# Performance work log

Measured on AMD Instinct MI355X. Metric: run time of the kernel, lower is better.

Reference implementation:

```python
import jax, jax.numpy as jnp
import numpy as np

EPS = 1e-3  # keras BatchNormalization default epsilon

def _spatial_shift(x):
    # x: [B, T, N, C]; channel c is circularly rolled along N by (c % N)
    B, T, N, C = x.shape
    shifts = np.arange(C) % N                      # [C]
    pos = np.arange(N)[:, None]                    # [N,1]
    # tf.roll(shift=s) moves element j to (j+s) % N, i.e. out[j] = in[(j - s) % N]
    gather_idx = (pos - shifts[None, :]) % N       # [N, C]
    return x[:, :, gather_idx, np.arange(C)]       # advanced indexing -> [B,T,N,C]

def setup_inputs() -> dict:
    key = jax.random.key(0)
    k1, k2, k3 = jax.random.split(key, 3)
    B, T, N, C_in, F = 8, 64, 21, 128, 256
    x = jax.random.normal(k1, (B, T, N, C_in), dtype=jnp.float32)
    W = jax.random.normal(k2, (C_in, F), dtype=jnp.float32) * (1.0 / np.sqrt(C_in))
    b = jnp.zeros((F,), dtype=jnp.float32)
    gamma = jnp.ones((F,), dtype=jnp.float32)
    beta = jnp.zeros((F,), dtype=jnp.float32)
    return {"x": x, "W": W, "b": b, "gamma": gamma, "beta": beta}

def reference(x, W, b, gamma, beta):
    # per-channel circular shift along N
    xs = _spatial_shift(x)                               # [B,T,N,C]
    # 1x1 conv == matmul over channel dim
    y = jnp.einsum('btnc,cf->btnf', xs, W) + b           # [B,T,N,F]
    # BatchNormalization with training=True: batch statistics over B,T,N
    mean = jnp.mean(y, axis=(0, 1, 2))
    var = jnp.var(y, axis=(0, 1, 2))
    y = (y - mean) * jax.lax.rsqrt(var + EPS) * gamma + beta
    return jax.nn.relu(y)
```

## Files before the change

### kernel.cpp

```cpp
#include <hip/hip_runtime.h>
#include <stdint.h>


#define NPOS 21
#define CIN  128
#define FOUT 256
#define BT   512
#define M_TOTAL 10752
#define BN_EPS 1e-3f
#define AROW 136

typedef short v8s __attribute__((ext_vector_type(8)));
typedef float v4f __attribute__((ext_vector_type(4)));

__device__ __forceinline__ uint16_t f2bf_rne(float f) {
    uint32_t u = __builtin_bit_cast(uint32_t, f);
    u += 0x7FFFu + ((u >> 16) & 1u);
    return (uint16_t)(u >> 16);
}

__global__ __launch_bounds__(256) void k_prep(const float* __restrict__ W,
                                              float* __restrict__ ws)
{
    const int t = threadIdx.x;
    if (blockIdx.x == 0) { ws[t] = 0.0f; ws[256 + t] = 0.0f; }

    uint4* dst = (uint4*)(ws + 1024);
    #pragma unroll
    for (int it = 0; it < 4; it++) {
        int q   = (blockIdx.x * 4 + it) * 256 + t;
        int l   = q & 63;
        int ks  = (q >> 6) & 3;
        int nt  = q >> 8;
        int kb  = ks * 32 + (l >> 4) * 8;
        int col = nt * 16 + (l & 15);
        uint32_t d[4];
        #pragma unroll
        for (int p = 0; p < 4; p++) {
            uint32_t lo = f2bf_rne(W[(size_t)(kb + 2 * p    ) * FOUT + col]);
            uint32_t hi = f2bf_rne(W[(size_t)(kb + 2 * p + 1) * FOUT + col]);
            d[p] = lo | (hi << 16);
        }
        dst[q] = make_uint4(d[0], d[1], d[2], d[3]);
    }
}

__global__ __launch_bounds__(256) void k_conv(const float* __restrict__ x,
                                              float* __restrict__ y,
                                              float* ws)
{
    __shared__ uint16_t asB[32 * AROW];
    __shared__ float sumL[FOUT], sqL[FOUT];

    const int bt = blockIdx.x;
    const int t  = threadIdx.x;

    for (int i = t; i < 704; i += 256) {
        int r  = 21 + (i >> 6);
        int c2 = (i & 63) << 1;
        *(uint32_t*)&asB[r * AROW + c2] = 0u;
    }
    const float* xin = x + (size_t)bt * (NPOS * CIN);
    for (int i = t; i < NPOS * CIN; i += 256) {
        float v = xin[i];
        int r = i >> 7;
        int c = i & (CIN - 1);
        int s = c % NPOS;
        int n = r + s; if (n >= NPOS) n -= NPOS;
        asB[n * AROW + c] = f2bf_rne(v);
    }
    __syncthreads();

    const int w     = t >> 6;
    const int l     = t & 63;
    const int row16 = l & 15;
    const int koct  = l >> 4;

    const uint4* wsw = (const uint4*)(ws + 1024);
    v8s bfr[4][4];
    #pragma unroll
    for (int nt = 0; nt < 4; nt++)
        #pragma unroll
        for (int ks = 0; ks < 4; ks++) {
            uint4 u = wsw[(((w * 4 + nt) * 4 + ks) << 6) + l];
            bfr[nt][ks] = __builtin_bit_cast(v8s, u);
        }

    float s4[4] = {0.f, 0.f, 0.f, 0.f};
    float q4[4] = {0.f, 0.f, 0.f, 0.f};
    float* yout = y + (size_t)bt * (NPOS * FOUT) + w * 64;

    #pragma unroll
    for (int m = 0; m < 2; m++) {
        v8s afr[4];
        #pragma unroll
        for (int ks = 0; ks < 4; ks++)
            afr[ks] = *(const v8s*)&asB[(m * 16 + row16) * AROW + ks * 32 + koct * 8];

        v4f acc[4];
        #pragma unroll
        for (int nt = 0; nt < 4; nt++) acc[nt] = (v4f){0.f, 0.f, 0.f, 0.f};

        #pragma unroll
        for (int ks = 0; ks < 4; ks++)
            #pragma unroll
            for (int nt = 0; nt < 4; nt++)
                acc[nt] = __builtin_amdgcn_mfma_f32_16x16x32_bf16(
                              afr[ks], bfr[nt][ks], acc[nt], 0, 0, 0);

        #pragma unroll
        for (int nt = 0; nt < 4; nt++) {
            #pragma unroll
            for (int rg = 0; rg < 4; rg++) {
                float v = acc[nt][rg];
                int gr = m * 16 + koct * 4 + rg;
                if (gr < NPOS)
                    yout[(size_t)gr * FOUT + nt * 16 + row16] = v;
                s4[nt] += v;
                q4[nt] += v * v;
            }
        }
    }

    #pragma unroll
    for (int nt = 0; nt < 4; nt++) {
        float s = s4[nt], q = q4[nt];
        s += __shfl_xor(s, 16); s += __shfl_xor(s, 32);
        q += __shfl_xor(q, 16); q += __shfl_xor(q, 32);
        if (l < 16) {
            sumL[w * 64 + nt * 16 + l] = s;
            sqL [w * 64 + nt * 16 + l] = q;
        }
    }
    __syncthreads();
    atomicAdd(ws + t, sumL[t]);
    atomicAdd(ws + FOUT + t, sqL[t]);
}

#define BN_BLOCKS 1344

__global__ __launch_bounds__(256) void k_bnapply(float* __restrict__ y,
                                                 const float* __restrict__ ws,
                                                 const float* __restrict__ gamma,
                                                 const float* __restrict__ beta)
{
    const int t  = threadIdx.x;
    const int fb = (t & 63) << 2;
    const float4 sm = *(const float4*)(ws + fb);
    const float4 sq = *(const float4*)(ws + FOUT + fb);
    const float4 gm = *(const float4*)(gamma + fb);
    const float4 be = *(const float4*)(beta + fb);
    const float invM = 1.0f / (float)M_TOTAL;

    float sc[4], bs[4];
    {
        float m0 = sm.x * invM, m1 = sm.y * invM, m2 = sm.z * invM, m3 = sm.w * invM;
        float v0 = fmaf(-m0, m0, sq.x * invM);
        float v1 = fmaf(-m1, m1, sq.y * invM);
        float v2 = fmaf(-m2, m2, sq.z * invM);
        float v3 = fmaf(-m3, m3, sq.w * invM);
        sc[0] = rsqrtf(v0 + BN_EPS) * gm.x;  bs[0] = be.x - m0 * sc[0];
        sc[1] = rsqrtf(v1 + BN_EPS) * gm.y;  bs[1] = be.y - m1 * sc[1];
        sc[2] = rsqrtf(v2 + BN_EPS) * gm.z;  bs[2] = be.z - m2 * sc[2];
        sc[3] = rsqrtf(v3 + BN_EPS) * gm.w;  bs[3] = be.w - m3 * sc[3];
    }

    float4* y4 = (float4*)y;
    #pragma unroll
    for (int it = 0; it < 2; it++) {
        int g = blockIdx.x * 512 + it * 256 + t;
        float4 v = y4[g];
        v.x = fmaxf(fmaf(v.x, sc[0], bs[0]), 0.0f);
        v.y = fmaxf(fmaf(v.y, sc[1], bs[1]), 0.0f);
        v.z = fmaxf(fmaf(v.z, sc[2], bs[2]), 0.0f);
        v.w = fmaxf(fmaf(v.w, sc[3], bs[3]), 0.0f);
        y4[g] = v;
    }
}

extern "C" __global__ void SpatialShiftConvBlock_71923522339050_kernel() {}

extern "C" void kernel_launch(void* const* d_in, const int* in_sizes, int n_in,
                              void* d_out, int out_size, void* d_ws, size_t ws_size,
                              hipStream_t stream) {
    float* y  = (float*)d_out;
    float* ws = (float*)d_ws;
    k_prep<<<4, 256, 0, stream>>>((const float*)d_in[1], ws);
    k_conv<<<BT, 256, 0, stream>>>((const float*)d_in[0], y, ws);
    k_bnapply<<<BN_BLOCKS, 256, 0, stream>>>(y, ws,
                                             (const float*)d_in[3], (const float*)d_in[4]);
}
```

Measured before the change: 91.37 us.

## Fuse conv, batch-stat reduction and BN apply into one kernel with grid barrier

Merges the weight prep, conv and BN-apply kernels into a single kernel. Each block converts W to bf16 fragments directly from global memory, keeps its conv accumulators in registers, and publishes partial sums via atomics. A software grid-wide barrier (atomic counter spin) then lets every block read the global statistics and write normalized ReLU output once. This removes the intermediate y write/read round-trip and two launches, but relies on all 512 blocks being co-resident and duplicates the W conversion in every block.

Measured after the change: 125.6 us. +37.5%, slower.

```diff
diff --git a/kernel.cpp b/kernel.cpp
--- a/kernel.cpp
+++ b/kernel.cpp
@@ -19,38 +19,16 @@
     return (uint16_t)(u >> 16);
 }
 
-__global__ __launch_bounds__(256) void k_prep(const float* __restrict__ W,
-                                              float* __restrict__ ws)
-{
-    const int t = threadIdx.x;
-    if (blockIdx.x == 0) { ws[t] = 0.0f; ws[256 + t] = 0.0f; }
-
-    uint4* dst = (uint4*)(ws + 1024);
-    #pragma unroll
-    for (int it = 0; it < 4; it++) {
-        int q   = (blockIdx.x * 4 + it) * 256 + t;
-        int l   = q & 63;
-        int ks  = (q >> 6) & 3;
-        int nt  = q >> 8;
-        int kb  = ks * 32 + (l >> 4) * 8;
-        int col = nt * 16 + (l & 15);
-        uint32_t d[4];
-        #pragma unroll
-        for (int p = 0; p < 4; p++) {
-            uint32_t lo = f2bf_rne(W[(size_t)(kb + 2 * p    ) * FOUT + col]);
-            uint32_t hi = f2bf_rne(W[(size_t)(kb + 2 * p + 1) * FOUT + col]);
-            d[p] = lo | (hi << 16);
-        }
-        dst[q] = make_uint4(d[0], d[1], d[2], d[3]);
-    }
-}
-
-__global__ __launch_bounds__(256) void k_conv(const float* __restrict__ x,
-                                              float* __restrict__ y,
-                                              float* ws)
+__global__ __launch_bounds__(256, 2) void k_fused(const float* __restrict__ x,
+                                                  const float* __restrict__ W,
+                                                  const float* __restrict__ gamma,
+                                                  const float* __restrict__ beta,
+                                                  float* __restrict__ y,
+                                                  float* ws)
 {
     __shared__ uint16_t asB[32 * AROW];
-    __shared__ float sumL[FOUT], sqL[FOUT];
+    __shared__ float scL[FOUT];
+    __shared__ float bsL[FOUT];
 
     const int bt = blockIdx.x;
     const int t  = threadIdx.x;
@@ -69,26 +47,37 @@
         int n = r + s; if (n >= NPOS) n -= NPOS;
         asB[n * AROW + c] = f2bf_rne(v);
     }
-    __syncthreads();
 
     const int w     = t >> 6;
     const int l     = t & 63;
     const int row16 = l & 15;
     const int koct  = l >> 4;
 
-    const uint4* wsw = (const uint4*)(ws + 1024);
     v8s bfr[4][4];
     #pragma unroll
-    for (int nt = 0; nt < 4; nt++)
+    for (int nt = 0; nt < 4; nt++) {
+        const int col = (w * 4 + nt) * 16 + row16;
         #pragma unroll
         for (int ks = 0; ks < 4; ks++) {
-            uint4 u = wsw[(((w * 4 + nt) * 4 + ks) << 6) + l];
+            const int kb = ks * 32 + koct * 8;
+            uint32_t d[4];
+            #pragma unroll
+            for (int p = 0; p < 4; p++) {
+                uint32_t lo = f2bf_rne(W[(size_t)(kb + 2 * p    ) * FOUT + col]);
+                uint32_t hi = f2bf_rne(W[(size_t)(kb + 2 * p + 1) * FOUT + col]);
+                d[p] = lo | (hi << 16);
+            }
+            uint4 u = make_uint4(d[0], d[1], d[2], d[3]);
             bfr[nt][ks] = __builtin_bit_cast(v8s, u);
         }
+    }
+    __syncthreads();
 
-    float s4[4] = {0.f, 0.f, 0.f, 0.f};
-    float q4[4] = {0.f, 0.f, 0.f, 0.f};
-    float* yout = y + (size_t)bt * (NPOS * FOUT) + w * 64;
+    v4f acc[2][4];
+    #pragma unroll
+    for (int m = 0; m < 2; m++)
+        #pragma unroll
+        for (int nt = 0; nt < 4; nt++) acc[m][nt] = (v4f){0.f, 0.f, 0.f, 0.f};
 
     #pragma unroll
     for (int m = 0; m < 2; m++) {
@@ -96,85 +85,75 @@
         #pragma unroll
         for (int ks = 0; ks < 4; ks++)
             afr[ks] = *(const v8s*)&asB[(m * 16 + row16) * AROW + ks * 32 + koct * 8];
-
-        v4f acc[4];
-        #pragma unroll
-        for (int nt = 0; nt < 4; nt++) acc[nt] = (v4f){0.f, 0.f, 0.f, 0.f};
-
         #pragma unroll
         for (int ks = 0; ks < 4; ks++)
             #pragma unroll
             for (int nt = 0; nt < 4; nt++)
-                acc[nt] = __builtin_amdgcn_mfma_f32_16x16x32_bf16(
-                              afr[ks], bfr[nt][ks], acc[nt], 0, 0, 0);
-
-        #pragma unroll
-        for (int nt = 0; nt < 4; nt++) {
-            #pragma unroll
-            for (int rg = 0; rg < 4; rg++) {
-                float v = acc[nt][rg];
-                int gr = m * 16 + koct * 4 + rg;
-                if (gr < NPOS)
-                    yout[(size_t)gr * FOUT + nt * 16 + row16] = v;
-                s4[nt] += v;
-                q4[nt] += v * v;
-            }
-        }
+                acc[m][nt] = __builtin_amdgcn_mfma_f32_16x16x32_bf16(
+                                 afr[ks], bfr[nt][ks], acc[m][nt], 0, 0, 0);
     }
 
     #pragma unroll
     for (int nt = 0; nt < 4; nt++) {
-        float s = s4[nt], q = q4[nt];
+        float s = 0.f, q = 0.f;
+        #pragma unroll
+        for (int m = 0; m < 2; m++)
+            #pragma unroll
+            for (int rg = 0; rg < 4; rg++) {
+                float v = acc[m][nt][rg];
+                s += v; q += v * v;
+            }
         s += __shfl_xor(s, 16); s += __shfl_xor(s, 32);
         q += __shfl_xor(q, 16); q += __shfl_xor(q, 32);
         if (l < 16) {
-            sumL[w * 64 + nt * 16 + l] = s;
-            sqL [w * 64 + nt * 16 + l] = q;
+            scL[w * 64 + nt * 16 + l] = s;
+            bsL[w * 64 + nt * 16 + l] = q;
         }
     }
     __syncthreads();
-    atomicAdd(ws + t, sumL[t]);
-    atomicAdd(ws + FOUT + t, sqL[t]);
-}
+    atomicAdd(ws + t, scL[t]);
+    atomicAdd(ws + FOUT + t, bsL[t]);
+    __threadfence();
+    __syncthreads();
 
-#define BN_BLOCKS 1344
+    if (t == 0) {
+        atomicAdd((unsigned int*)(ws + 512), 1u);
+        while (__hip_atomic_load((unsigned int*)(ws + 512),
+                                 __ATOMIC_RELAXED, __HIP_MEMORY_SCOPE_AGENT)
+               < (unsigned int)gridDim.x)
+            __builtin_amdgcn_s_sleep(2);
+    }
+    __syncthreads();
 
-__global__ __launch_bounds__(256) void k_bnapply(float* __restrict__ y,
-                                                 const float* __restrict__ ws,
-                                                 const float* __restrict__ gamma,
-                                                 const float* __restrict__ beta)
-{
-    const int t  = threadIdx.x;
-    const int fb = (t & 63) << 2;
-    const float4 sm = *(const float4*)(ws + fb);
-    const float4 sq = *(const float4*)(ws + FOUT + fb);
-    const float4 gm = *(const float4*)(gamma + fb);
-    const float4 be = *(const float4*)(beta + fb);
-    const float invM = 1.0f / (float)M_TOTAL;
+    {
+        float s = __hip_atomic_load(ws + t, __ATOMIC_RELAXED,
+                                    __HIP_MEMORY_SCOPE_AGENT);
+        float q = __hip_atomic_load(ws + FOUT + t, __ATOMIC_RELAXED,
+                                    __HIP_MEMORY_SCOPE_AGENT);
+        const float invM = 1.0f / (float)M_TOTAL;
+        float mean = s * invM;
+        float var  = fmaf(-mean, mean, q * invM);
+        float sc   = rsqrtf(var + BN_EPS) * gamma[t];
+        scL[t] = sc;
+        bsL[t] = beta[t] - mean * sc;
+    }
+    __syncthreads();
 
-    float sc[4], bs[4];
-    {
-        float m0 = sm.x * invM, m1 = sm.y * invM, m2 = sm.z * invM, m3 = sm.w * invM;
-        float v0 = fmaf(-m0, m0, sq.x * invM);
-        float v1 = fmaf(-m1, m1, sq.y * invM);
-        float v2 = fmaf(-m2, m2, sq.z * invM);
-        float v3 = fmaf(-m3, m3, sq.w * invM);
-        sc[0] = rsqrtf(v0 + BN_EPS) * gm.x;  bs[0] = be.x - m0 * sc[0];
-        sc[1] = rsqrtf(v1 + BN_EPS) * gm.y;  bs[1] = be.y - m1 * sc[1];
-        sc[2] = rsqrtf(v2 + BN_EPS) * gm.z;  bs[2] = be.z - m2 * sc[2];
-        sc[3] = rsqrtf(v3 + BN_EPS) * gm.w;  bs[3] = be.w - m3 * sc[3];
-    }
-
-    float4* y4 = (float4*)y;
+    float* yout = y + (size_t)bt * (NPOS * FOUT);
     #pragma unroll
-    for (int it = 0; it < 2; it++) {
-        int g = blockIdx.x * 512 + it * 256 + t;
-        float4 v = y4[g];
-        v.x = fmaxf(fmaf(v.x, sc[0], bs[0]), 0.0f);
-        v.y = fmaxf(fmaf(v.y, sc[1], bs[1]), 0.0f);
-        v.z = fmaxf(fmaf(v.z, sc[2], bs[2]), 0.0f);
-        v.w = fmaxf(fmaf(v.w, sc[3], bs[3]), 0.0f);
-        y4[g] = v;
+    for (int nt = 0; nt < 4; nt++) {
+        const int ch = w * 64 + nt * 16 + row16;
+        const float sc = scL[ch];
+        const float bs = bsL[ch];
+        #pragma unroll
+        for (int m = 0; m < 2; m++)
+            #pragma unroll
+            for (int rg = 0; rg < 4; rg++) {
+                int gr = m * 16 + koct * 4 + rg;
+                if (gr < NPOS)
+                    yout[(size_t)gr * FOUT + ch] =
+                        fmaxf(fmaf(acc[m][nt][rg], sc, bs), 0.0f);
+            }
     }
 }
 
@@ -185,8 +164,8 @@
                               hipStream_t stream) {
     float* y  = (float*)d_out;
     float* ws = (float*)d_ws;
-    k_prep<<<4, 256, 0, stream>>>((const float*)d_in[1], ws);
-    k_conv<<<BT, 256, 0, stream>>>((const float*)d_in[0], y, ws);
-    k_bnapply<<<BN_BLOCKS, 256, 0, stream>>>(y, ws,
-                                             (const float*)d_in[3], (const float*)d_in[4]);
+    hipMemsetAsync(ws, 0, 516 * sizeof(float), stream);
+    k_fused<<<BT, 256, 0, stream>>>((const float*)d_in[0], (const float*)d_in[1],
+                                    (const float*)d_in[3], (const float*)d_in[4],
+                                    y, ws);
 }
```

## Split conv output features across two blocks per row group and widen prep grid

Applied to the files above, without the earlier changes.

The conv kernel now launches two blocks per (b,t) slice, each computing half of the 256 output features, so each wave holds fewer B fragments. This doubles grid parallelism on a 256-CU device. In exchange, the shifted input tile is loaded and converted twice. The weight-prep kernel uses 16 blocks with one fragment per thread instead of 4 blocks looping, and the B-fragment loads are moved ahead of the LDS barrier to overlap with the input staging. Atomics per block are halved, though the total number of atomics stays the same.

Measured after the change: 91.41 us. Within noise of the previous version (+0.0%).

```diff
diff --git a/kernel.cpp b/kernel.cpp
--- a/kernel.cpp
+++ b/kernel.cpp
@@ -9,6 +9,7 @@
 #define M_TOTAL 10752
 #define BN_EPS 1e-3f
 #define AROW 136
+#define WSFRAG 1024
 
 typedef short v8s __attribute__((ext_vector_type(8)));
 typedef float v4f __attribute__((ext_vector_type(4)));
@@ -23,26 +24,23 @@
                                               float* __restrict__ ws)
 {
     const int t = threadIdx.x;
-    if (blockIdx.x == 0) { ws[t] = 0.0f; ws[256 + t] = 0.0f; }
+    const int b = blockIdx.x;
+    if (b < 2) ws[b * 256 + t] = 0.0f;
 
-    uint4* dst = (uint4*)(ws + 1024);
+    const int q  = b * 256 + t;
+    const int l  = q & 63;
+    const int ks = (q >> 6) & 3;
+    const int nt = q >> 8;
+    const int kb = ks * 32 + (l >> 4) * 8;
+    const int col = nt * 16 + (l & 15);
+    uint32_t d[4];
     #pragma unroll
-    for (int it = 0; it < 4; it++) {
-        int q   = (blockIdx.x * 4 + it) * 256 + t;
-        int l   = q & 63;
-        int ks  = (q >> 6) & 3;
-        int nt  = q >> 8;
-        int kb  = ks * 32 + (l >> 4) * 8;
-        int col = nt * 16 + (l & 15);
-        uint32_t d[4];
-        #pragma unroll
-        for (int p = 0; p < 4; p++) {
-            uint32_t lo = f2bf_rne(W[(size_t)(kb + 2 * p    ) * FOUT + col]);
-            uint32_t hi = f2bf_rne(W[(size_t)(kb + 2 * p + 1) * FOUT + col]);
-            d[p] = lo | (hi << 16);
-        }
-        dst[q] = make_uint4(d[0], d[1], d[2], d[3]);
+    for (int p = 0; p < 4; p++) {
+        uint32_t lo = f2bf_rne(W[(size_t)(kb + 2 * p    ) * FOUT + col]);
+        uint32_t hi = f2bf_rne(W[(size_t)(kb + 2 * p + 1) * FOUT + col]);
+        d[p] = lo | (hi << 16);
     }
+    ((uint4*)(ws + WSFRAG))[q] = make_uint4(d[0], d[1], d[2], d[3]);
 }
 
 __global__ __launch_bounds__(256) void k_conv(const float* __restrict__ x,
@@ -50,9 +48,10 @@
                                               float* ws)
 {
     __shared__ uint16_t asB[32 * AROW];
-    __shared__ float sumL[FOUT], sqL[FOUT];
+    __shared__ float scL[128], sqL[128];
 
-    const int bt = blockIdx.x;
+    const int bt = blockIdx.x >> 1;
+    const int fh = blockIdx.x & 1;
     const int t  = threadIdx.x;
 
     for (int i = t; i < 704; i += 256) {
@@ -69,26 +68,30 @@
         int n = r + s; if (n >= NPOS) n -= NPOS;
         asB[n * AROW + c] = f2bf_rne(v);
     }
-    __syncthreads();
 
     const int w     = t >> 6;
     const int l     = t & 63;
     const int row16 = l & 15;
     const int koct  = l >> 4;
 
-    const uint4* wsw = (const uint4*)(ws + 1024);
-    v8s bfr[4][4];
+    const uint4* wsw = (const uint4*)(ws + WSFRAG);
+    v8s bfr[2][4];
     #pragma unroll
-    for (int nt = 0; nt < 4; nt++)
+    for (int nt = 0; nt < 2; nt++) {
+        const int ntg = fh * 8 + w * 2 + nt;
         #pragma unroll
         for (int ks = 0; ks < 4; ks++) {
-            uint4 u = wsw[(((w * 4 + nt) * 4 + ks) << 6) + l];
+            uint4 u = wsw[(((ntg << 2) + ks) << 6) + l];
             bfr[nt][ks] = __builtin_bit_cast(v8s, u);
         }
+    }
+    __syncthreads();
 
-    float s4[4] = {0.f, 0.f, 0.f, 0.f};
-    float q4[4] = {0.f, 0.f, 0.f, 0.f};
-    float* yout = y + (size_t)bt * (NPOS * FOUT) + w * 64;
+    v4f acc[2][2];
+    #pragma unroll
+    for (int m = 0; m < 2; m++)
+        #pragma unroll
+        for (int nt = 0; nt < 2; nt++) acc[m][nt] = (v4f){0.f, 0.f, 0.f, 0.f};
 
     #pragma unroll
     for (int m = 0; m < 2; m++) {
@@ -96,45 +99,39 @@
         #pragma unroll
         for (int ks = 0; ks < 4; ks++)
             afr[ks] = *(const v8s*)&asB[(m * 16 + row16) * AROW + ks * 32 + koct * 8];
-
-        v4f acc[4];
-        #pragma unroll
-        for (int nt = 0; nt < 4; nt++) acc[nt] = (v4f){0.f, 0.f, 0.f, 0.f};
-
         #pragma unroll
         for (int ks = 0; ks < 4; ks++)
             #pragma unroll
-            for (int nt = 0; nt < 4; nt++)
-                acc[nt] = __builtin_amdgcn_mfma_f32_16x16x32_bf16(
-                              afr[ks], bfr[nt][ks], acc[nt], 0, 0, 0);
+            for (int nt = 0; nt < 2; nt++)
+                acc[m][nt] = __builtin_amdgcn_mfma_f32_16x16x32_bf16(
+                                 afr[ks], bfr[nt][ks], acc[m][nt], 0, 0, 0);
+    }
 
+    float* yout = y + (size_t)bt * (NPOS * FOUT) + fh * 128 + w * 32;
+    #pragma unroll
+    for (int nt = 0; nt < 2; nt++) {
+        float s = 0.f, q = 0.f;
         #pragma unroll
-        for (int nt = 0; nt < 4; nt++) {
+        for (int m = 0; m < 2; m++)
             #pragma unroll
             for (int rg = 0; rg < 4; rg++) {
-                float v = acc[nt][rg];
+                float v = acc[m][nt][rg];
+                s += v; q += v * v;
                 int gr = m * 16 + koct * 4 + rg;
                 if (gr < NPOS)
                     yout[(size_t)gr * FOUT + nt * 16 + row16] = v;
-                s4[nt] += v;
-                q4[nt] += v * v;
             }
-        }
-    }
-
-    #pragma unroll
-    for (int nt = 0; nt < 4; nt++) {
-        float s = s4[nt], q = q4[nt];
         s += __shfl_xor(s, 16); s += __shfl_xor(s, 32);
         q += __shfl_xor(q, 16); q += __shfl_xor(q, 32);
         if (l < 16) {
-            sumL[w * 64 + nt * 16 + l] = s;
-            sqL [w * 64 + nt * 16 + l] = q;
+            scL[w * 32 + nt * 16 + l] = s;
+            sqL[w * 32 + nt * 16 + l] = q;
         }
     }
     __syncthreads();
-    atomicAdd(ws + t, sumL[t]);
-    atomicAdd(ws + FOUT + t, sqL[t]);
+
+    if (t < 128) atomicAdd(ws + fh * 128 + t, scL[t]);
+    else         atomicAdd(ws + 256 + fh * 128 + (t - 128), sqL[t - 128]);
 }
 
 #define BN_BLOCKS 1344
@@ -185,8 +182,8 @@
                               hipStream_t stream) {
     float* y  = (float*)d_out;
     float* ws = (float*)d_ws;
-    k_prep<<<4, 256, 0, stream>>>((const float*)d_in[1], ws);
-    k_conv<<<BT, 256, 0, stream>>>((const float*)d_in[0], y, ws);
+    k_prep<<<16, 256, 0, stream>>>((const float*)d_in[1], ws);
+    k_conv<<<2 * BT, 256, 0, stream>>>((const float*)d_in[0], y, ws);
     k_bnapply<<<BN_BLOCKS, 256, 0, stream>>>(y, ws,
                                              (const float*)d_in[3], (const float*)d_in[4]);
 }
```
